# Optimization experiments

Hardware: AMD Instinct MI355X
Metric: run time of the kernel (lower is better)

The kernel has to match this reference:

```python
import jax, jax.numpy as jnp
import numpy as np

B, N, DIM = 4, 4096, 1024
HEADS, DIM_HEAD = 16, 64
DIM_INNER = HEADS * DIM_HEAD
ATTN_SCALE = 8.0
EPS = 1e-12  # F.normalize default eps


def setup_inputs() -> dict:
    key = jax.random.key(0)
    k1, k2, k3, k4, k5 = jax.random.split(key, 5)
    x = jax.random.normal(k1, (B, N, DIM), dtype=jnp.float32)
    gamma = jnp.ones((DIM,), dtype=jnp.float32)
    # stored as (in, out) so forward is x @ w
    w_qkv = jax.random.normal(k2, (DIM, 3 * DIM_INNER), dtype=jnp.float32) * (DIM ** -0.5)
    temperature = jnp.ones((HEADS, 1, 1), dtype=jnp.float32)
    w_out = jax.random.normal(k3, (DIM_INNER, DIM), dtype=jnp.float32) * (DIM_INNER ** -0.5)
    return {"x": x, "gamma": gamma, "w_qkv": w_qkv, "temperature": temperature, "w_out": w_out}


def _l2norm(t):
    # F.normalize(t, dim=-1): t / max(||t||_2, eps)
    n = jnp.linalg.norm(t, axis=-1, keepdims=True)
    return t / jnp.maximum(n, EPS)


def reference(x, gamma, w_qkv, temperature, w_out):
    b, n, dim = x.shape
    # RMSNorm: F.normalize(x, dim=-1) * sqrt(dim) * gamma
    xn = _l2norm(x) * (dim ** 0.5) * gamma
    # QKV projection -> qkv b h d n
    qkv = (xn @ w_qkv).reshape(b, n, 3, HEADS, DIM_HEAD)
    qkv = qkv.transpose(2, 0, 3, 4, 1)  # (3, b, h, d, n)
    q, k, v = qkv[0], qkv[1], qkv[2]
    # l2-normalize q, k over the sequence (last) axis; temperature-scale q
    q = _l2norm(q) * jnp.exp(temperature)  # temperature: (h,1,1) broadcast
    k = _l2norm(k)
    # cross-covariance attention over the small channel dim d
    sim = jnp.einsum('bhdn,bhen->bhde', q, k) * ATTN_SCALE
    attn = jax.nn.softmax(sim, axis=-1)
    out = jnp.einsum('bhde,bhen->bhdn', attn, v)
    # b h d n -> b n (h d), then out projection
    out = out.transpose(0, 3, 1, 2).reshape(b, n, DIM_INNER)
    return out @ w_out
```

## Files before the change

### kernel.cpp

```cpp
#include <hip/hip_runtime.h>
#include <stdint.h>

typedef unsigned short u16;
typedef unsigned int u32;
typedef __attribute__((ext_vector_type(8))) __bf16 bf16x8;
typedef __attribute__((ext_vector_type(4))) float f32x4;

#define M_TOT 16384
#define DIMX  1024

__device__ __forceinline__ u16 f2b(float f) {
  u32 u = __builtin_bit_cast(u32, f);
  u32 r = (u + 0x7fffu + ((u >> 16) & 1u)) >> 16;
  return (u16)r;
}

__device__ __forceinline__ void gl2lds16(const void* g, void* l) {
  __builtin_amdgcn_global_load_lds((const __attribute__((address_space(1))) void*)g,
                                   (__attribute__((address_space(3))) void*)l,
                                   16, 0, 0);
}

__global__ __launch_bounds__(256) void k_rms(const float* __restrict__ x,
                                             const float* __restrict__ gamma,
                                             u16* __restrict__ xn) {
  int row = blockIdx.x;
  int t = threadIdx.x;
  const float4* xr = (const float4*)(x + (size_t)row * DIMX);
  float4 v = xr[t];
  float ss = v.x * v.x + v.y * v.y + v.z * v.z + v.w * v.w;
#pragma unroll
  for (int o = 32; o > 0; o >>= 1) ss += __shfl_xor(ss, o, 64);
  __shared__ float wss[4];
  int w = t >> 6;
  if ((t & 63) == 0) wss[w] = ss;
  __syncthreads();
  float tot = wss[0] + wss[1] + wss[2] + wss[3];
  float scale = 32.0f / fmaxf(sqrtf(tot), 1e-12f);
  float4 g = ((const float4*)gamma)[t];
  ushort4 o4;
  o4.x = f2b(v.x * scale * g.x);
  o4.y = f2b(v.y * scale * g.y);
  o4.z = f2b(v.z * scale * g.z);
  o4.w = f2b(v.w * scale * g.w);
  ((ushort4*)xn)[(size_t)row * 256 + t] = o4;
}

__global__ __launch_bounds__(256) void k_castT(const float* __restrict__ in,
                                               u16* __restrict__ out, int Rr, int Cc) {
  __shared__ float tile[32][33];
  int c0 = blockIdx.x * 32, r0 = blockIdx.y * 32;
  int tx = threadIdx.x, ty = threadIdx.y;
#pragma unroll
  for (int i = 0; i < 4; i++)
    tile[ty + i * 8][tx] = in[(size_t)(r0 + ty + i * 8) * Cc + c0 + tx];
  __syncthreads();
#pragma unroll
  for (int i = 0; i < 4; i++)
    out[(size_t)(c0 + ty + i * 8) * Rr + r0 + tx] = f2b(tile[tx][ty + i * 8]);
}

template<bool SWAP>
__device__ __forceinline__ void gemm_core128(const u16* __restrict__ Ag,
                                             const u16* __restrict__ Bg,
                                             u16* Al, u16* Bl,
                                             int t, f32x4 (&acc)[4][4]) {
  int w = t >> 6, lane = t & 63;
  int r16 = lane & 15, q = lane >> 4;
  int wi = w >> 1, wj = w & 1;
  int swz = (r16 >> 1) & 3;
  int qs8 = ((q ^ swz) & 3) * 8;
  for (int k0 = 0; k0 < 1024; k0 += 64) {
    __syncthreads();
#pragma unroll
    for (int h = 0; h < 2; h++) {
#pragma unroll
      for (int r = 0; r < 2; r++) {
        int chunk = (r << 8) + t;
        int row = chunk >> 2;
        int cc = (chunk & 3) ^ ((row >> 1) & 3);
        u16* la = Al + h * 4096 + ((r << 8) + (w << 6)) * 8;
        u16* lb = Bl + h * 4096 + ((r << 8) + (w << 6)) * 8;
        gl2lds16(Ag + (size_t)row * 1024 + k0 + h * 32 + cc * 8, la);
        gl2lds16(Bg + (size_t)row * 1024 + k0 + h * 32 + cc * 8, lb);
      }
    }
    __syncthreads();
#pragma unroll
    for (int h = 0; h < 2; h++) {
      bf16x8 af[4], bfr[4];
#pragma unroll
      for (int i = 0; i < 4; i++) {
        af[i]  = *(const bf16x8*)(Al + h * 4096 + (wi * 64 + i * 16 + r16) * 32 + qs8);
        bfr[i] = *(const bf16x8*)(Bl + h * 4096 + (wj * 64 + i * 16 + r16) * 32 + qs8);
      }
#pragma unroll
      for (int i = 0; i < 4; i++)
#pragma unroll
        for (int j = 0; j < 4; j++)
          acc[i][j] = SWAP
            ? __builtin_amdgcn_mfma_f32_16x16x32_bf16(bfr[j], af[i], acc[i][j], 0, 0, 0)
            : __builtin_amdgcn_mfma_f32_16x16x32_bf16(af[i], bfr[j], acc[i][j], 0, 0, 0);
    }
  }
}

__global__ __launch_bounds__(256) void k_gemm1(const u16* __restrict__ A,
                                               const u16* __restrict__ Bt,
                                               u16* __restrict__ qkT,
                                               u16* __restrict__ vmat,
                                               float* __restrict__ sumsq) {
  __shared__ u16 Al[2 * 4096];
  __shared__ u16 Bl[2 * 4096];
  int l = blockIdx.x;
  int xcd = l & 7, idx = l >> 3;
  int m0 = (xcd * 16 + (idx & 15)) * 128;
  int n0 = (idx >> 4) * 128;
  int t = threadIdx.x, lane = t & 63, w = t >> 6;
  int wi = w >> 1, wj = w & 1;
  int r16 = lane & 15, q = lane >> 4;
  f32x4 acc[4][4] = {};
  if (n0 < 2048) {
    gemm_core128<false>(A + (size_t)m0 * 1024, Bt + (size_t)n0 * 1024, Al, Bl, t, acc);
    int b = m0 >> 12;
#pragma unroll
    for (int j = 0; j < 4; j++) {
      int c = n0 + wj * 64 + j * 16 + r16;
      float colss = 0.f;
#pragma unroll
      for (int i = 0; i < 4; i++) {
        f32x4 a = acc[i][j];
        colss += a.x * a.x + a.y * a.y + a.z * a.z + a.w * a.w;
        int m = m0 + wi * 64 + i * 16 + q * 4;
        ushort4 o4;
        o4.x = f2b(a.x); o4.y = f2b(a.y); o4.z = f2b(a.z); o4.w = f2b(a.w);
        *(ushort4*)(qkT + (size_t)c * M_TOT + m) = o4;
      }
      colss += __shfl_xor(colss, 16, 64);
      colss += __shfl_xor(colss, 32, 64);
      if (lane < 16) atomicAdd(&sumsq[b * 2048 + c], colss);
    }
  } else {
    gemm_core128<true>(A + (size_t)m0 * 1024, Bt + (size_t)n0 * 1024, Al, Bl, t, acc);
    int vc0 = n0 - 2048;
#pragma unroll
    for (int i = 0; i < 4; i++) {
      int m = m0 + wi * 64 + i * 16 + r16;
#pragma unroll
      for (int j = 0; j < 4; j++) {
        int c = vc0 + wj * 64 + j * 16 + q * 4;
        f32x4 a = acc[i][j];
        ushort4 o4;
        o4.x = f2b(a.x); o4.y = f2b(a.y); o4.z = f2b(a.z); o4.w = f2b(a.w);
        *(ushort4*)(vmat + (size_t)m * 1024 + c) = o4;
      }
    }
  }
}

__global__ __launch_bounds__(256) void k_attn_s(const u16* __restrict__ qkT,
                                                float* __restrict__ Spart) {
  int g = blockIdx.x, split = blockIdx.y;
  int t = threadIdx.x, lane = t & 63, w = t >> 6;
  int bh = g * 4 + w;
  int b = bh >> 4, h = bh & 15;
  int r16 = lane & 15, q = lane >> 4;
  const u16* qbase = qkT + (size_t)(h * 64) * M_TOT + b * 4096;
  const u16* kbase = qkT + (size_t)(1024 + h * 64) * M_TOT + b * 4096;
  f32x4 acc[4][4] = {};
#pragma unroll
  for (int it = 0; it < 8; it++) {
    int kk = split * 256 + it * 32 + q * 8;
    bf16x8 af[4], bfr[4];
#pragma unroll
    for (int i = 0; i < 4; i++) af[i] = *(const bf16x8*)(qbase + (size_t)(i * 16 + r16) * M_TOT + kk);
#pragma unroll
    for (int j = 0; j < 4; j++) bfr[j] = *(const bf16x8*)(kbase + (size_t)(j * 16 + r16) * M_TOT + kk);
#pragma unroll
    for (int i = 0; i < 4; i++)
#pragma unroll
      for (int j = 0; j < 4; j++)
        acc[i][j] = __builtin_amdgcn_mfma_f32_16x16x32_bf16(bfr[j], af[i], acc[i][j], 0, 0, 0);
  }
  float* Sp = Spart + ((size_t)split * 64 + bh) * 4096;
#pragma unroll
  for (int i = 0; i < 4; i++) {
    int d = i * 16 + r16;
#pragma unroll
    for (int j = 0; j < 4; j++) {
      int e = j * 16 + q * 4;
      *(f32x4*)(Sp + d * 64 + e) = acc[i][j];
    }
  }
}

__global__ __launch_bounds__(64) void k_softmax(const float* __restrict__ Spart,
                                                const float* __restrict__ sumsq,
                                                const float* __restrict__ temp,
                                                u16* __restrict__ PT) {
  int bh = blockIdx.x;
  int b = bh >> 4, h = bh & 15;
  int d = threadIdx.x;
  __shared__ float rnk[64];
  rnk[d] = 1.0f / fmaxf(sqrtf(sumsq[b * 2048 + 1024 + h * 64 + d]), 1e-12f);
  __syncthreads();
  float nq = sqrtf(sumsq[b * 2048 + h * 64 + d]);
  float qs = 8.0f * __expf(temp[h]) / fmaxf(nq, 1e-12f);
  const float* Sp = Spart + (size_t)bh * 4096 + d * 64;
  float vals[64];
#pragma unroll
  for (int e = 0; e < 64; e += 4) {
    f32x4 v = {};
#pragma unroll
    for (int s = 0; s < 16; s++)
      v += *(const f32x4*)(Sp + (size_t)s * 64 * 4096 + e);
    vals[e + 0] = v.x; vals[e + 1] = v.y; vals[e + 2] = v.z; vals[e + 3] = v.w;
  }
  float mx = -3.0e38f;
#pragma unroll
  for (int e = 0; e < 64; e++) {
    float v = vals[e] * qs * rnk[e];
    vals[e] = v;
    mx = fmaxf(mx, v);
  }
  float sum = 0.f;
#pragma unroll
  for (int e = 0; e < 64; e++) {
    float v = __expf(vals[e] - mx);
    vals[e] = v;
    sum += v;
  }
  float inv = 1.0f / sum;
#pragma unroll
  for (int e = 0; e < 64; e++)
    PT[((size_t)bh * 64 + e) * 64 + d] = f2b(vals[e] * inv);
}

__global__ __launch_bounds__(256) void k_m(const u16* __restrict__ woT,
                                           const u16* __restrict__ PT,
                                           u16* __restrict__ MT) {
  int bh = blockIdx.x;
  int b = bh >> 4, h = bh & 15;
  int o0 = blockIdx.y * 128;
  int t = threadIdx.x, lane = t & 63, w = t >> 6;
  int r16 = lane & 15, q = lane >> 4;
  const u16* pbase = PT + (size_t)bh * 4096;
  f32x4 acc[2][4] = {};
#pragma unroll
  for (int ks = 0; ks < 2; ks++) {
    int kk = ks * 32 + q * 8;
    bf16x8 af[2], bfr[4];
#pragma unroll
    for (int i = 0; i < 2; i++)
      af[i] = *(const bf16x8*)(woT + (size_t)(o0 + w * 32 + i * 16 + r16) * 1024 + h * 64 + kk);
#pragma unroll
    for (int j = 0; j < 4; j++)
      bfr[j] = *(const bf16x8*)(pbase + (size_t)(j * 16 + r16) * 64 + kk);
#pragma unroll
    for (int i = 0; i < 2; i++)
#pragma unroll
      for (int j = 0; j < 4; j++)
        acc[i][j] = __builtin_amdgcn_mfma_f32_16x16x32_bf16(af[i], bfr[j], acc[i][j], 0, 0, 0);
  }
  u16* dst = MT + (size_t)b * 1024 * 1024;
#pragma unroll
  for (int i = 0; i < 2; i++) {
    int o = o0 + w * 32 + i * 16 + q * 4;
#pragma unroll
    for (int j = 0; j < 4; j++) {
      int e = h * 64 + j * 16 + r16;
      f32x4 a = acc[i][j];
      dst[(size_t)(o + 0) * 1024 + e] = f2b(a.x);
      dst[(size_t)(o + 1) * 1024 + e] = f2b(a.y);
      dst[(size_t)(o + 2) * 1024 + e] = f2b(a.z);
      dst[(size_t)(o + 3) * 1024 + e] = f2b(a.w);
    }
  }
}

__global__ __launch_bounds__(256) void k_gemm2(const u16* __restrict__ A,
                                               const u16* __restrict__ Bt,
                                               float* __restrict__ C) {
  __shared__ u16 Al[2 * 4096];
  __shared__ u16 Bl[2 * 4096];
  int l = blockIdx.x;
  int xcd = l & 7, idx = l >> 3;
  int m0 = (xcd * 16 + (idx & 15)) * 128;
  int n0 = (idx >> 4) * 128;
  int b = m0 >> 12;
  const u16* Bb = Bt + (size_t)b * 1024 * 1024;
  int t = threadIdx.x, lane = t & 63, w = t >> 6;
  int wi = w >> 1, wj = w & 1;
  int r16 = lane & 15, q = lane >> 4;
  f32x4 acc[4][4] = {};
  gemm_core128<true>(A + (size_t)m0 * 1024, Bb + (size_t)n0 * 1024, Al, Bl, t, acc);
#pragma unroll
  for (int i = 0; i < 4; i++) {
    int m = m0 + wi * 64 + i * 16 + r16;
#pragma unroll
    for (int j = 0; j < 4; j++) {
      int c = n0 + wj * 64 + j * 16 + q * 4;
      *(f32x4*)(C + (size_t)m * 1024 + c) = acc[i][j];
    }
  }
}

extern "C" void kernel_launch(void* const* d_in, const int* in_sizes, int n_in,
                              void* d_out, int out_size, void* d_ws, size_t ws_size,
                              hipStream_t stream) {
  const float* x     = (const float*)d_in[0];
  const float* gamma = (const float*)d_in[1];
  const float* wqkv  = (const float*)d_in[2];
  const float* temp  = (const float*)d_in[3];
  const float* wout  = (const float*)d_in[4];
  float* out = (float*)d_out;

  char* ws = (char*)d_ws;
  size_t off = 0;
  u16* xn = (u16*)(ws + off);    off += (size_t)M_TOT * 1024 * 2;
  u16* wqT = (u16*)(ws + off);   off += (size_t)3072 * 1024 * 2;
  u16* woT = (u16*)(ws + off);   off += (size_t)1024 * 1024 * 2;
  u16* qkT = (u16*)(ws + off);   off += (size_t)2048 * M_TOT * 2;
  u16* vmat = (u16*)(ws + off);  off += (size_t)M_TOT * 1024 * 2;
  float* sumsq = (float*)(ws + off); off += (size_t)4 * 2048 * 4;
  u16* PT = (u16*)(ws + off);    off += (size_t)64 * 64 * 64 * 2;
  u16* MT = (u16*)(ws + off);    off += (size_t)4 * 1024 * 1024 * 2;

  float* Spart = (float*)xn;

  hipMemsetAsync((void*)sumsq, 0, (size_t)4 * 2048 * 4, stream);

  k_rms<<<16384, 256, 0, stream>>>(x, gamma, xn);
  dim3 cb(32, 8);
  k_castT<<<dim3(3072 / 32, 1024 / 32), cb, 0, stream>>>(wqkv, wqT, 1024, 3072);
  k_castT<<<dim3(1024 / 32, 1024 / 32), cb, 0, stream>>>(wout, woT, 1024, 1024);
  k_gemm1<<<3072, 256, 0, stream>>>(xn, wqT, qkT, vmat, sumsq);
  k_attn_s<<<dim3(16, 16), 256, 0, stream>>>(qkT, Spart);
  k_softmax<<<64, 64, 0, stream>>>(Spart, sumsq, temp, PT);
  k_m<<<dim3(64, 8), 256, 0, stream>>>(woT, PT, MT);
  k_gemm2<<<1024, 256, 0, stream>>>(vmat, MT, out);
}
```

Measured before the change: 361.1 us.

## Replace 128x128 GEMM core with double-buffered 256x256 8-wave pipelined core

Both large GEMMs now use a 256x256 tile computed by 512 threads (8 waves), with double-buffered LDS and a 64-wide K step. Each quarter of the next K tile is prefetched via global_load_lds while MFMAs run on the current one, coordinated by explicit waitcnt and barriers, with s_setprio raising priority around the MFMA blocks. The larger tile raises data reuse and the prefetch is meant to hide global load latency that the old single-buffered loop exposed. In exchange it needs 128 KB of LDS and more registers per thread, and launches far fewer blocks (768 and 256), which risks load imbalance across CUs.

```diff
diff --git a/kernel.cpp b/kernel.cpp
--- a/kernel.cpp
+++ b/kernel.cpp
@@ -60,78 +60,161 @@
     out[(size_t)(c0 + ty + i * 8) * Rr + r0 + tx] = f2b(tile[tx][ty + i * 8]);
 }
 
+
 template<bool SWAP>
-__device__ __forceinline__ void gemm_core128(const u16* __restrict__ Ag,
+__device__ __forceinline__ f32x4 mf(bf16x8 a, bf16x8 b, f32x4 c) {
+  return SWAP ? __builtin_amdgcn_mfma_f32_16x16x32_bf16(b, a, c, 0, 0, 0)
+              : __builtin_amdgcn_mfma_f32_16x16x32_bf16(a, b, c, 0, 0, 0);
+}
+
+__device__ __forceinline__ void stage_half(const u16* __restrict__ g,
+                                           u16* dst, int t, int k0) {
+#pragma unroll
+  for (int r = 0; r < 2; r++) {
+    int chunk = r * 512 + t;
+    int row = chunk >> 3;
+    int cc = (chunk & 7) ^ (row & 7);
+    gl2lds16(g + (size_t)row * 1024 + (k0 + cc * 8),
+             dst + (r * 512 + (t >> 6) * 64) * 8);
+  }
+}
+
+template<bool SWAP>
+__device__ __forceinline__ void gemm_core256(const u16* __restrict__ Ag,
                                              const u16* __restrict__ Bg,
-                                             u16* Al, u16* Bl,
-                                             int t, f32x4 (&acc)[4][4]) {
-  int w = t >> 6, lane = t & 63;
+                                             u16* lds, int t, f32x4 (&acc)[8][4]) {
+  const int lane = t & 63;
+  const int r16 = lane & 15, q = lane >> 4;
+  const int wr = (t >> 6) >> 2, wc = (t >> 6) & 3;
+  const int s0 = (q ^ (r16 & 7)) * 8;
+  const int arow = wr * 16 + r16;
+  const int brow = wc * 16 + r16;
+
+  stage_half(Ag,              lds + 0 * 8192, t, 0);
+  stage_half(Bg,              lds + 2 * 8192, t, 0);
+  stage_half(Bg + 128 * 1024, lds + 3 * 8192, t, 0);
+  stage_half(Ag + 128 * 1024, lds + 1 * 8192, t, 0);
+  asm volatile("s_waitcnt vmcnt(4)" ::: "memory");
+  __builtin_amdgcn_s_barrier();
+
+  bf16x8 af[4][2], bl[2][2], bh[2][2];
+#pragma unroll 1
+  for (int tt = 0; tt < 16; tt++) {
+    const int bo = (tt & 1) << 15;
+    const int nb = bo ^ 32768;
+    const int k1 = ((tt + 1) & 15) << 6;
+    const u16* A0 = lds + bo;
+    const u16* A1 = lds + bo + 8192;
+    const u16* B0 = lds + bo + 16384;
+    const u16* B1 = lds + bo + 24576;
+
+#pragma unroll
+    for (int i = 0; i < 4; i++) {
+      af[i][0] = *(const bf16x8*)(A0 + (i * 32 + arow) * 64 + s0);
+      af[i][1] = *(const bf16x8*)(A0 + (i * 32 + arow) * 64 + (s0 ^ 32));
+    }
+#pragma unroll
+    for (int j = 0; j < 2; j++) {
+      bl[j][0] = *(const bf16x8*)(B0 + (j * 64 + brow) * 64 + s0);
+      bl[j][1] = *(const bf16x8*)(B0 + (j * 64 + brow) * 64 + (s0 ^ 32));
+    }
+    stage_half(Ag, lds + nb + 0 * 8192, t, k1);
+    asm volatile("s_waitcnt lgkmcnt(8)" ::: "memory");
+    __builtin_amdgcn_s_barrier();
+    asm volatile("s_waitcnt lgkmcnt(0)" ::: "memory");
+    __builtin_amdgcn_s_setprio(1);
+#pragma unroll
+    for (int kq = 0; kq < 2; kq++)
+#pragma unroll
+      for (int i = 0; i < 4; i++)
+#pragma unroll
+        for (int j = 0; j < 2; j++)
+          acc[i][j] = mf<SWAP>(af[i][kq], bl[j][kq], acc[i][j]);
+    __builtin_amdgcn_s_setprio(0);
+    asm volatile("s_waitcnt vmcnt(4)" ::: "memory");
+    __builtin_amdgcn_s_barrier();
+
+#pragma unroll
+    for (int j = 0; j < 2; j++) {
+      bh[j][0] = *(const bf16x8*)(B1 + (j * 64 + brow) * 64 + s0);
+      bh[j][1] = *(const bf16x8*)(B1 + (j * 64 + brow) * 64 + (s0 ^ 32));
+    }
+    stage_half(Bg, lds + nb + 2 * 8192, t, k1);
+    __builtin_amdgcn_s_barrier();
+    asm volatile("s_waitcnt lgkmcnt(0)" ::: "memory");
+    __builtin_amdgcn_s_setprio(1);
+#pragma unroll
+    for (int kq = 0; kq < 2; kq++)
+#pragma unroll
+      for (int i = 0; i < 4; i++)
+#pragma unroll
+        for (int j = 0; j < 2; j++)
+          acc[i][2 + j] = mf<SWAP>(af[i][kq], bh[j][kq], acc[i][2 + j]);
+    __builtin_amdgcn_s_setprio(0);
+    asm volatile("s_waitcnt vmcnt(4)" ::: "memory");
+    __builtin_amdgcn_s_barrier();
+
+#pragma unroll
+    for (int i = 0; i < 4; i++) {
+      af[i][0] = *(const bf16x8*)(A1 + (i * 32 + arow) * 64 + s0);
+      af[i][1] = *(const bf16x8*)(A1 + (i * 32 + arow) * 64 + (s0 ^ 32));
+    }
+    stage_half(Bg + 128 * 1024, lds + nb + 3 * 8192, t, k1);
+    __builtin_amdgcn_s_barrier();
+    asm volatile("s_waitcnt lgkmcnt(0)" ::: "memory");
+    __builtin_amdgcn_s_setprio(1);
+#pragma unroll
+    for (int kq = 0; kq < 2; kq++)
+#pragma unroll
+      for (int i = 0; i < 4; i++)
+#pragma unroll
+        for (int j = 0; j < 2; j++)
+          acc[4 + i][j] = mf<SWAP>(af[i][kq], bl[j][kq], acc[4 + i][j]);
+    __builtin_amdgcn_s_setprio(0);
+    __builtin_amdgcn_s_barrier();
+
+    stage_half(Ag + 128 * 1024, lds + nb + 1 * 8192, t, k1);
+    __builtin_amdgcn_s_barrier();
+    __builtin_amdgcn_s_setprio(1);
+#pragma unroll
+    for (int kq = 0; kq < 2; kq++)
+#pragma unroll
+      for (int i = 0; i < 4; i++)
+#pragma unroll
+        for (int j = 0; j < 2; j++)
+          acc[4 + i][2 + j] = mf<SWAP>(af[i][kq], bh[j][kq], acc[4 + i][2 + j]);
+    __builtin_amdgcn_s_setprio(0);
+    asm volatile("s_waitcnt vmcnt(4)" ::: "memory");
+    __builtin_amdgcn_s_barrier();
+  }
+}
+
+__global__ __launch_bounds__(512, 2) void k_gemm1(const u16* __restrict__ A,
+                                                  const u16* __restrict__ Bt,
+                                                  u16* __restrict__ qkT,
+                                                  u16* __restrict__ vmat,
+                                                  float* __restrict__ sumsq) {
+  __shared__ u16 lds[8 * 8192];
+  int l = blockIdx.x;
+  int wg = (l & 7) * 96 + (l >> 3);
+  int mt = wg & 63, nt = wg >> 6;
+  int m0 = mt * 256, n0 = nt * 256;
+  int t = threadIdx.x, lane = t & 63;
   int r16 = lane & 15, q = lane >> 4;
-  int wi = w >> 1, wj = w & 1;
-  int swz = (r16 >> 1) & 3;
-  int qs8 = ((q ^ swz) & 3) * 8;
-  for (int k0 = 0; k0 < 1024; k0 += 64) {
-    __syncthreads();
-#pragma unroll
-    for (int h = 0; h < 2; h++) {
-#pragma unroll
-      for (int r = 0; r < 2; r++) {
-        int chunk = (r << 8) + t;
-        int row = chunk >> 2;
-        int cc = (chunk & 3) ^ ((row >> 1) & 3);
-        u16* la = Al + h * 4096 + ((r << 8) + (w << 6)) * 8;
-        u16* lb = Bl + h * 4096 + ((r << 8) + (w << 6)) * 8;
-        gl2lds16(Ag + (size_t)row * 1024 + k0 + h * 32 + cc * 8, la);
-        gl2lds16(Bg + (size_t)row * 1024 + k0 + h * 32 + cc * 8, lb);
-      }
-    }
-    __syncthreads();
-#pragma unroll
-    for (int h = 0; h < 2; h++) {
-      bf16x8 af[4], bfr[4];
-#pragma unroll
-      for (int i = 0; i < 4; i++) {
-        af[i]  = *(const bf16x8*)(Al + h * 4096 + (wi * 64 + i * 16 + r16) * 32 + qs8);
-        bfr[i] = *(const bf16x8*)(Bl + h * 4096 + (wj * 64 + i * 16 + r16) * 32 + qs8);
-      }
-#pragma unroll
-      for (int i = 0; i < 4; i++)
-#pragma unroll
-        for (int j = 0; j < 4; j++)
-          acc[i][j] = SWAP
-            ? __builtin_amdgcn_mfma_f32_16x16x32_bf16(bfr[j], af[i], acc[i][j], 0, 0, 0)
-            : __builtin_amdgcn_mfma_f32_16x16x32_bf16(af[i], bfr[j], acc[i][j], 0, 0, 0);
-    }
-  }
-}
-
-__global__ __launch_bounds__(256) void k_gemm1(const u16* __restrict__ A,
-                                               const u16* __restrict__ Bt,
-                                               u16* __restrict__ qkT,
-                                               u16* __restrict__ vmat,
-                                               float* __restrict__ sumsq) {
-  __shared__ u16 Al[2 * 4096];
-  __shared__ u16 Bl[2 * 4096];
-  int l = blockIdx.x;
-  int xcd = l & 7, idx = l >> 3;
-  int m0 = (xcd * 16 + (idx & 15)) * 128;
-  int n0 = (idx >> 4) * 128;
-  int t = threadIdx.x, lane = t & 63, w = t >> 6;
-  int wi = w >> 1, wj = w & 1;
-  int r16 = lane & 15, q = lane >> 4;
-  f32x4 acc[4][4] = {};
+  int wr = (t >> 6) >> 2, wc = (t >> 6) & 3;
+  f32x4 acc[8][4] = {};
   if (n0 < 2048) {
-    gemm_core128<false>(A + (size_t)m0 * 1024, Bt + (size_t)n0 * 1024, Al, Bl, t, acc);
+    gemm_core256<false>(A + (size_t)m0 * 1024, Bt + (size_t)n0 * 1024, lds, t, acc);
     int b = m0 >> 12;
 #pragma unroll
     for (int j = 0; j < 4; j++) {
-      int c = n0 + wj * 64 + j * 16 + r16;
+      int c = n0 + j * 64 + wc * 16 + r16;
       float colss = 0.f;
 #pragma unroll
-      for (int i = 0; i < 4; i++) {
+      for (int i = 0; i < 8; i++) {
         f32x4 a = acc[i][j];
         colss += a.x * a.x + a.y * a.y + a.z * a.z + a.w * a.w;
-        int m = m0 + wi * 64 + i * 16 + q * 4;
+        int m = m0 + i * 32 + wr * 16 + q * 4;
         ushort4 o4;
         o4.x = f2b(a.x); o4.y = f2b(a.y); o4.z = f2b(a.z); o4.w = f2b(a.w);
         *(ushort4*)(qkT + (size_t)c * M_TOT + m) = o4;
@@ -141,14 +224,14 @@
       if (lane < 16) atomicAdd(&sumsq[b * 2048 + c], colss);
     }
   } else {
-    gemm_core128<true>(A + (size_t)m0 * 1024, Bt + (size_t)n0 * 1024, Al, Bl, t, acc);
+    gemm_core256<true>(A + (size_t)m0 * 1024, Bt + (size_t)n0 * 1024, lds, t, acc);
     int vc0 = n0 - 2048;
 #pragma unroll
-    for (int i = 0; i < 4; i++) {
-      int m = m0 + wi * 64 + i * 16 + r16;
+    for (int i = 0; i < 8; i++) {
+      int m = m0 + i * 32 + wr * 16 + r16;
 #pragma unroll
       for (int j = 0; j < 4; j++) {
-        int c = vc0 + wj * 64 + j * 16 + q * 4;
+        int c = vc0 + j * 64 + wc * 16 + q * 4;
         f32x4 a = acc[i][j];
         ushort4 o4;
         o4.x = f2b(a.x); o4.y = f2b(a.y); o4.z = f2b(a.z); o4.w = f2b(a.w);
@@ -278,28 +361,27 @@
   }
 }
 
-__global__ __launch_bounds__(256) void k_gemm2(const u16* __restrict__ A,
-                                               const u16* __restrict__ Bt,
-                                               float* __restrict__ C) {
-  __shared__ u16 Al[2 * 4096];
-  __shared__ u16 Bl[2 * 4096];
+__global__ __launch_bounds__(512, 2) void k_gemm2(const u16* __restrict__ A,
+                                                  const u16* __restrict__ Bt,
+                                                  float* __restrict__ C) {
+  __shared__ u16 lds[8 * 8192];
   int l = blockIdx.x;
-  int xcd = l & 7, idx = l >> 3;
-  int m0 = (xcd * 16 + (idx & 15)) * 128;
-  int n0 = (idx >> 4) * 128;
+  int wg = (l & 7) * 32 + (l >> 3);
+  int mt = wg & 63, nt = wg >> 6;
+  int m0 = mt * 256, n0 = nt * 256;
   int b = m0 >> 12;
   const u16* Bb = Bt + (size_t)b * 1024 * 1024;
-  int t = threadIdx.x, lane = t & 63, w = t >> 6;
-  int wi = w >> 1, wj = w & 1;
+  int t = threadIdx.x, lane = t & 63;
   int r16 = lane & 15, q = lane >> 4;
-  f32x4 acc[4][4] = {};
-  gemm_core128<true>(A + (size_t)m0 * 1024, Bb + (size_t)n0 * 1024, Al, Bl, t, acc);
-#pragma unroll
-  for (int i = 0; i < 4; i++) {
-    int m = m0 + wi * 64 + i * 16 + r16;
+  int wr = (t >> 6) >> 2, wc = (t >> 6) & 3;
+  f32x4 acc[8][4] = {};
+  gemm_core256<true>(A + (size_t)m0 * 1024, Bb + (size_t)n0 * 1024, lds, t, acc);
+#pragma unroll
+  for (int i = 0; i < 8; i++) {
+    int m = m0 + i * 32 + wr * 16 + r16;
 #pragma unroll
     for (int j = 0; j < 4; j++) {
-      int c = n0 + wj * 64 + j * 16 + q * 4;
+      int c = n0 + j * 64 + wc * 16 + q * 4;
       *(f32x4*)(C + (size_t)m * 1024 + c) = acc[i][j];
     }
   }
@@ -334,9 +416,9 @@
   dim3 cb(32, 8);
   k_castT<<<dim3(3072 / 32, 1024 / 32), cb, 0, stream>>>(wqkv, wqT, 1024, 3072);
   k_castT<<<dim3(1024 / 32, 1024 / 32), cb, 0, stream>>>(wout, woT, 1024, 1024);
-  k_gemm1<<<3072, 256, 0, stream>>>(xn, wqT, qkT, vmat, sumsq);
+  k_gemm1<<<768, 512, 0, stream>>>(xn, wqT, qkT, vmat, sumsq);
   k_attn_s<<<dim3(16, 16), 256, 0, stream>>>(qkT, Spart);
   k_softmax<<<64, 64, 0, stream>>>(Spart, sumsq, temp, PT);
   k_m<<<dim3(64, 8), 256, 0, stream>>>(woT, PT, MT);
-  k_gemm2<<<1024, 256, 0, stream>>>(vmat, MT, out);
-}
+  k_gemm2<<<1024 / 4, 512, 0, stream>>>(vmat, MT, out);
+}
```

New measurement: 338.0 us. 1.07x faster.
